# Kernel tuning notes

Hardware: AMD Instinct MI355X
Metric: run time of the kernel (lower is better)

The kernel has to match this reference:

```python
import jax, jax.numpy as jnp
import numpy as np

N, E, F = 20000, 160000, 128
H, C1, C2 = 4, 128, 256
G, NCLS = 64, 10


def setup_inputs() -> dict:
    key = jax.random.key(0)
    ks = jax.random.split(key, 14)
    s = 0.05
    inp = {
        "x": jax.random.normal(ks[0], (N, F), jnp.float32),
        "edge_index": jax.random.randint(ks[1], (2, E), 0, N, dtype=jnp.int32),
        "batch": ((jnp.arange(N, dtype=jnp.int32) * G) // N),  # sorted graph ids, all 64 graphs non-empty
        # GATConv 1: in=128 -> 128 per head, heads=4, concat -> 512
        "W1": jax.random.normal(ks[2], (F, H * C1), jnp.float32) * s,
        "att_src1": jax.random.normal(ks[3], (H, C1), jnp.float32) * s,
        "att_dst1": jax.random.normal(ks[4], (H, C1), jnp.float32) * s,
        "b1": jnp.zeros((H * C1,), jnp.float32),
        # GATConv 2: in=512 -> 256, heads=1, concat=False
        "W2": jax.random.normal(ks[5], (H * C1, C2), jnp.float32) * s,
        "att_src2": jax.random.normal(ks[6], (1, C2), jnp.float32) * s,
        "att_dst2": jax.random.normal(ks[7], (1, C2), jnp.float32) * s,
        "b2": jnp.zeros((C2,), jnp.float32),
        # fc head
        "fc1_w": jax.random.normal(ks[8], (C2, 64), jnp.float32) * s,
        "fc1_b": jnp.zeros((64,), jnp.float32),
        "fc2_w": jax.random.normal(ks[9], (64, NCLS), jnp.float32) * s,
        "fc2_b": jnp.zeros((NCLS,), jnp.float32),
    }
    return inp


def gat_conv(x, src, dst, W, att_src, att_dst, bias, concat):
    """PyG GATConv: per-edge attention + segment softmax over dst + scatter-add."""
    n = x.shape[0]
    h_, c_ = att_src.shape
    h = (x @ W).reshape(n, h_, c_)                    # [N,H,C]
    a_src = jnp.einsum('nhc,hc->nh', h, att_src)       # [N,H]
    a_dst = jnp.einsum('nhc,hc->nh', h, att_dst)       # [N,H]
    e = jax.nn.leaky_relu(a_src[src] + a_dst[dst], negative_slope=0.2)  # [Etot,H]
    e_max = jax.ops.segment_max(e, dst, num_segments=n)
    ee = jnp.exp(e - e_max[dst])
    denom = jax.ops.segment_sum(ee, dst, num_segments=n)
    alpha = ee / denom[dst]                            # [Etot,H]
    out = jax.ops.segment_sum(h[src] * alpha[:, :, None], dst, num_segments=n)  # [N,H,C]
    out = out.reshape(n, h_ * c_) if concat else out.mean(axis=1)
    return out + bias


def reference(x, edge_index, batch, W1, att_src1, att_dst1, b1,
              W2, att_src2, att_dst2, b2, fc1_w, fc1_b, fc2_w, fc2_b):
    n = x.shape[0]
    # to_undirected: both directions; plus self-loops (GATConv add_self_loops=True)
    loops = jnp.arange(n, dtype=edge_index.dtype)
    src = jnp.concatenate([edge_index[0], edge_index[1], loops])
    dst = jnp.concatenate([edge_index[1], edge_index[0], loops])
    h = gat_conv(x, src, dst, W1, att_src1, att_dst1, b1, concat=True)
    h = jax.nn.relu(h)
    h = gat_conv(h, src, dst, W2, att_src2, att_dst2, b2, concat=False)
    g = jax.ops.segment_max(h, batch, num_segments=G)  # global_max_pool
    g = jax.nn.relu(g @ fc1_w + fc1_b) @ fc2_w + fc2_b
    return jax.nn.log_softmax(g, axis=1)
```

## Files before the change

### kernel.cpp

```cpp
#include <hip/hip_runtime.h>
#include <math.h>

#define FDIM 128
#define HEADS 4
#define C1DIM 128
#define C2DIM 256
#define NGRAPH 64
#define NCLS 10

typedef __attribute__((ext_vector_type(8))) short short8;
typedef __attribute__((ext_vector_type(4))) float float4v;
typedef __attribute__((ext_vector_type(2))) float floatx2;

__device__ __forceinline__ unsigned short f2bf(float f) {
    unsigned u = __builtin_bit_cast(unsigned, f);
    unsigned r = (u + 0x7FFFu + ((u >> 16) & 1u)) >> 16;
    return (unsigned short)r;
}
__device__ __forceinline__ float bfu(unsigned short u) { return __builtin_bit_cast(float, (unsigned)u << 16); }
__device__ __forceinline__ float lrelu(float x) { return x > 0.f ? x : 0.2f * x; }
__device__ __forceinline__ float sel4(float a, float b, float c, float d, int hd) {
    return hd == 0 ? a : hd == 1 ? b : hd == 2 ? c : d;
}
__device__ __forceinline__ unsigned char f2fp8(float f) {
    return (unsigned char)(__builtin_amdgcn_cvt_pk_fp8_f32(f, f, 0, false) & 0xff);
}
__device__ __forceinline__ void fp8x8_dec(int2 r, float* f) {
    floatx2 p0 = __builtin_amdgcn_cvt_pk_f32_fp8(r.x, false);
    floatx2 p1 = __builtin_amdgcn_cvt_pk_f32_fp8(r.x, true);
    floatx2 p2 = __builtin_amdgcn_cvt_pk_f32_fp8(r.y, false);
    floatx2 p3 = __builtin_amdgcn_cvt_pk_f32_fp8(r.y, true);
    f[0] = p0.x; f[1] = p0.y; f[2] = p1.x; f[3] = p1.y;
    f[4] = p2.x; f[5] = p2.y; f[6] = p3.x; f[7] = p3.y;
}
__device__ __forceinline__ void fp8x4_dec(int r, float* f) {
    floatx2 p0 = __builtin_amdgcn_cvt_pk_f32_fp8(r, false);
    floatx2 p1 = __builtin_amdgcn_cvt_pk_f32_fp8(r, true);
    f[0] = p0.x; f[1] = p0.y; f[2] = p1.x; f[3] = p1.y;
}
__device__ __forceinline__ unsigned encf(float v) {
    unsigned b = __builtin_bit_cast(unsigned, v);
    return (b & 0x80000000u) ? ~b : (b | 0x80000000u);
}
__device__ __forceinline__ float decf(unsigned u) {
    unsigned b = (u & 0x80000000u) ? (u ^ 0x80000000u) : ~u;
    return __builtin_bit_cast(float, b);
}

__global__ __launch_bounds__(256) void prep_kernel(
        int* __restrict__ zero_base, int nzero_words,
        const float* __restrict__ x, unsigned short* __restrict__ xb, int n4,
        const float* __restrict__ W1, unsigned short* __restrict__ W1t,
        const float* __restrict__ W2, unsigned short* __restrict__ W2t,
        int ZB, int CB) {
    __shared__ float tile[32][33];
    int blk = blockIdx.x;
    if (blk < ZB) {
        int i = blk * 256 + threadIdx.x;
        if (i < nzero_words) zero_base[i] = 0;
        return;
    }
    blk -= ZB;
    if (blk < CB) {
        int i = blk * 256 + threadIdx.x;
        if (i < n4) {
            float4 v = ((const float4*)x)[i];
            ushort4 o;
            o.x = f2bf(v.x); o.y = f2bf(v.y); o.z = f2bf(v.z); o.w = f2bf(v.w);
            ((ushort4*)xb)[i] = o;
        }
        return;
    }
    blk -= CB;
    const float* W; unsigned short* Wt; int K, Nc, bx, by;
    if (blk < 64) {
        W = W1; Wt = W1t; K = 128; Nc = 512;
        bx = (blk & 15) * 32; by = (blk >> 4) * 32;
    } else {
        blk -= 64;
        W = W2; Wt = W2t; K = 512; Nc = 256;
        bx = (blk & 7) * 32; by = (blk >> 3) * 32;
    }
    int tx = threadIdx.x & 31, ty = threadIdx.x >> 5;
    #pragma unroll
    for (int r = 0; r < 32; r += 8)
        tile[ty + r][tx] = W[(size_t)(by + ty + r) * Nc + bx + tx];
    __syncthreads();
    #pragma unroll
    for (int r = 0; r < 32; r += 8)
        Wt[(size_t)(bx + ty + r) * K + by + tx] = f2bf(tile[tx][ty + r]);
}

__global__ void hist_kernel(const int* __restrict__ ei, int E, int* __restrict__ counts) {
    int i = blockIdx.x * blockDim.x + threadIdx.x;
    if (i >= 2 * E) return;
    int dst = (i < E) ? ei[E + i] : ei[i - E];
    atomicAdd(&counts[dst], 1);
}

__global__ __launch_bounds__(1024) void scan_kernel(int* __restrict__ counts_cursor,
                                                    int* __restrict__ ofs, int N) {
    __shared__ int part[1024];
    int t = threadIdx.x;
    int chunk = (N + 1023) / 1024;
    int b = t * chunk;
    int e = b + chunk; if (e > N) e = N;
    int s = 0;
    int i = b;
    if ((chunk & 3) == 0) {
        for (; i + 4 <= e; i += 4) {
            int4 v = *(const int4*)&counts_cursor[i];
            s += v.x + v.y + v.z + v.w;
        }
    }
    for (; i < e; ++i) s += counts_cursor[i];
    part[t] = s;
    __syncthreads();
    for (int o = 1; o < 1024; o <<= 1) {
        int v = (t >= o) ? part[t - o] : 0;
        __syncthreads();
        part[t] += v;
        __syncthreads();
    }
    int run = part[t] - s;
    i = b;
    if ((chunk & 3) == 0) {
        for (; i + 4 <= e; i += 4) {
            int4 c = *(const int4*)&counts_cursor[i];
            int4 o4;
            o4.x = run; run += c.x;
            o4.y = run; run += c.y;
            o4.z = run; run += c.z;
            o4.w = run; run += c.w;
            *(int4*)&ofs[i] = o4;
            counts_cursor[i]     = o4.x;
            counts_cursor[i + 1] = o4.y;
            counts_cursor[i + 2] = o4.z;
            counts_cursor[i + 3] = o4.w;
        }
    }
    for (; i < e; ++i) {
        int c = counts_cursor[i];
        ofs[i] = run;
        counts_cursor[i] = run;
        run += c;
    }
    if (t == 1023) ofs[N] = part[1023];
}

__global__ void scatter_kernel(const int* __restrict__ ei, int E,
                               int* __restrict__ cursor, int* __restrict__ esrc) {
    int i = blockIdx.x * blockDim.x + threadIdx.x;
    if (i >= 2 * E) return;
    int src = ei[i];
    int dst = (i < E) ? ei[E + i] : ei[i - E];
    int pos = atomicAdd(&cursor[dst], 1);
    esrc[pos] = src;
}

template<int MODE>
__global__ __launch_bounds__(256) void bgemm_kernel(
        const unsigned short* __restrict__ A,
        const unsigned short* __restrict__ Bt,
        unsigned char* __restrict__ Cout,
        const float* __restrict__ att_src,
        const float* __restrict__ att_dst,
        float* __restrict__ as_out,
        float* __restrict__ ad_out,
        int M, int N_, int K) {
    constexpr int BN = (MODE == 1) ? 128 : 256;
    constexpr int JW = BN / 32;
    constexpr int CPADB = BN + 16;
    constexpr int SMEMB = 4096 + BN * 64;
    __shared__ __align__(16) unsigned char smem[SMEMB];
    unsigned short* As = (unsigned short*)smem;
    unsigned short* Bs = (unsigned short*)(smem + 4096);
    __shared__ float sd_s[4][32];
    __shared__ float sd_d[4][32];
    const int t = threadIdx.x;
    const int lane = t & 63;
    const int wave = t >> 6;
    const int row0 = blockIdx.y * 64, col0 = blockIdx.x * BN;
    const int wr = (wave >> 1) * 32, wc = (wave & 1) * (BN / 2);
    float4v acc[2][JW] = {};
    for (int k0 = 0; k0 < K; k0 += 32) {
        {
            int i = t;
            int gr = row0 + (i >> 2); if (gr >= M) gr = M - 1;
            const unsigned short* gp = A + (size_t)gr * K + k0 + ((i & 3) << 3);
            __builtin_amdgcn_global_load_lds(
                (const __attribute__((address_space(1))) unsigned int*)gp,
                (__attribute__((address_space(3))) unsigned int*)&As[i * 8], 16, 0, 0);
        }
        #pragma unroll
        for (int c = 0; c < BN / 64; ++c) {
            int i = c * 256 + t;
            int gn = col0 + (i >> 2);
            const unsigned short* gp = Bt + (size_t)gn * K + k0 + ((i & 3) << 3);
            __builtin_amdgcn_global_load_lds(
                (const __attribute__((address_space(1))) unsigned int*)gp,
                (__attribute__((address_space(3))) unsigned int*)&Bs[i * 8], 16, 0, 0);
        }
        __syncthreads();
        short8 af[2], bfr[JW];
        #pragma unroll
        for (int i = 0; i < 2; ++i)
            af[i] = *(const short8*)&As[(wr + i * 16 + (lane & 15)) * 32 + (lane >> 4) * 8];
        #pragma unroll
        for (int j = 0; j < JW; ++j)
            bfr[j] = *(const short8*)&Bs[(wc + j * 16 + (lane & 15)) * 32 + (lane >> 4) * 8];
        #pragma unroll
        for (int i = 0; i < 2; ++i)
            #pragma unroll
            for (int j = 0; j < JW; ++j)
                acc[i][j] = __builtin_amdgcn_mfma_f32_16x16x32_bf16(af[i], bfr[j], acc[i][j], 0, 0, 0);
        __syncthreads();
    }
    float asv[JW], adv[JW];
    #pragma unroll
    for (int j = 0; j < JW; ++j) {
        int cc = col0 + wc + j * 16 + (lane & 15);
        asv[j] = att_src[cc];
        adv[j] = att_dst[cc];
    }
    #pragma unroll
    for (int i = 0; i < 2; ++i) {
        #pragma unroll
        for (int p = 0; p < 4; ++p) {
            int rr = wr + i * 16 + (lane >> 4) * 4 + p;
            float s = 0.f, d = 0.f;
            #pragma unroll
            for (int j = 0; j < JW; ++j) {
                smem[rr * CPADB + wc + j * 16 + (lane & 15)] = f2fp8(acc[i][j][p]);
                s += acc[i][j][p] * asv[j];
                d += acc[i][j][p] * adv[j];
            }
            #pragma unroll
            for (int o = 1; o <= 8; o <<= 1) { s += __shfl_xor(s, o); d += __shfl_xor(d, o); }
            if ((lane & 15) == 0) {
                int ridx = i * 16 + (lane >> 4) * 4 + p;
                sd_s[wave][ridx] = s;
                sd_d[wave][ridx] = d;
            }
        }
    }
    __syncthreads();
    #pragma unroll
    for (int it = 0; it < BN / 64; ++it) {
        int idx = it * 256 + t;
        int row = idx / (BN / 16), c16 = (idx % (BN / 16)) * 16;
        int grw = row0 + row;
        if (grw < M)
            *(int4*)&Cout[(size_t)grw * N_ + col0 + c16] = *(const int4*)&smem[row * CPADB + c16];
    }
    if ((wave & 1) == 0 && lane < 32) {
        float s = sd_s[wave][lane] + sd_s[wave + 1][lane];
        float d = sd_d[wave][lane] + sd_d[wave + 1][lane];
        int r = row0 + wr + lane;
        if (r < M) {
            if (MODE == 1) {
                as_out[r * 4 + blockIdx.x] = s;
                ad_out[r * 4 + blockIdx.x] = d;
            } else {
                as_out[r] = s;
                ad_out[r] = d;
            }
        }
    }
}

__global__ __launch_bounds__(256) void edge_agg1_kernel(
        const unsigned char* __restrict__ h1f8,
        const float4* __restrict__ as14,
        const float4* __restrict__ ad14,
        const int* __restrict__ ofs,
        const int* __restrict__ esrc,
        const float* __restrict__ b1,
        unsigned short* __restrict__ ho1b, int N) {
    __shared__ int sl_s[4][64];
    __shared__ __align__(16) float4 w_s[4][64];
    int wave = threadIdx.x >> 6, lane = threadIdx.x & 63;
    int node = blockIdx.x * 4 + wave;
    if (node >= N) return;
    int beg = ofs[node], end = ofs[node + 1];
    float4 asn = as14[node], adn = ad14[node];
    float w0 = __expf(lrelu(asn.x + adn.x));
    float w1 = __expf(lrelu(asn.y + adn.y));
    float w2 = __expf(lrelu(asn.z + adn.z));
    float w3 = __expf(lrelu(asn.w + adn.w));
    int hd = lane >> 4;
    int c0 = lane * 8;
    float wsh = sel4(w0, w1, w2, w3, hd);
    float acc[8];
    {
        int2 rs = *(const int2*)&h1f8[(size_t)node * 512 + c0];
        float f[8]; fp8x8_dec(rs, f);
        #pragma unroll
        for (int k = 0; k < 8; ++k) acc[k] = wsh * f[k];
    }
    float d0 = 0.f, d1 = 0.f, d2 = 0.f, d3 = 0.f;
    for (int cb = beg; cb < end; cb += 64) {
        int idx = cb + lane;
        int sl = esrc[idx < end ? idx : end - 1];
        float4 wl = make_float4(0.f, 0.f, 0.f, 0.f);
        if (idx < end) {
            float4 a = as14[sl];
            wl.x = __expf(lrelu(a.x + adn.x));
            wl.y = __expf(lrelu(a.y + adn.y));
            wl.z = __expf(lrelu(a.z + adn.z));
            wl.w = __expf(lrelu(a.w + adn.w));
            d0 += wl.x; d1 += wl.y; d2 += wl.z; d3 += wl.w;
        }
        sl_s[wave][lane] = sl;
        w_s[wave][lane] = wl;
        int jmax = end - cb; if (jmax > 64) jmax = 64;
        int j = 0;
        for (; j + 4 <= jmax; j += 4) {
            int s0 = sl_s[wave][j],     s1 = sl_s[wave][j + 1];
            int s2 = sl_s[wave][j + 2], s3 = sl_s[wave][j + 3];
            float u0 = ((const float*)&w_s[wave][j])[hd];
            float u1 = ((const float*)&w_s[wave][j + 1])[hd];
            float u2 = ((const float*)&w_s[wave][j + 2])[hd];
            float u3 = ((const float*)&w_s[wave][j + 3])[hd];
            int2 r0 = *(const int2*)&h1f8[(size_t)s0 * 512 + c0];
            int2 r1 = *(const int2*)&h1f8[(size_t)s1 * 512 + c0];
            int2 r2 = *(const int2*)&h1f8[(size_t)s2 * 512 + c0];
            int2 r3 = *(const int2*)&h1f8[(size_t)s3 * 512 + c0];
            float f0[8], f1[8], f2[8], f3[8];
            fp8x8_dec(r0, f0); fp8x8_dec(r1, f1); fp8x8_dec(r2, f2); fp8x8_dec(r3, f3);
            #pragma unroll
            for (int k = 0; k < 8; ++k)
                acc[k] += u0 * f0[k] + u1 * f1[k] + u2 * f2[k] + u3 * f3[k];
        }
        for (; j < jmax; ++j) {
            int s = sl_s[wave][j];
            float u = ((const float*)&w_s[wave][j])[hd];
            int2 r = *(const int2*)&h1f8[(size_t)s * 512 + c0];
            float f[8]; fp8x8_dec(r, f);
            #pragma unroll
            for (int k = 0; k < 8; ++k) acc[k] += u * f[k];
        }
    }
    #pragma unroll
    for (int o = 32; o > 0; o >>= 1) {
        d0 += __shfl_xor(d0, o); d1 += __shfl_xor(d1, o);
        d2 += __shfl_xor(d2, o); d3 += __shfl_xor(d3, o);
    }
    d0 += w0; d1 += w1; d2 += w2; d3 += w3;
    float dh = sel4(d0, d1, d2, d3, hd);
    float inv = 1.f / dh;
    float4 bA = *(const float4*)&b1[c0], bB = *(const float4*)&b1[c0 + 4];
    float v0 = fmaxf(acc[0] * inv + bA.x, 0.f), v1 = fmaxf(acc[1] * inv + bA.y, 0.f);
    float v2 = fmaxf(acc[2] * inv + bA.z, 0.f), v3 = fmaxf(acc[3] * inv + bA.w, 0.f);
    float v4 = fmaxf(acc[4] * inv + bB.x, 0.f), v5 = fmaxf(acc[5] * inv + bB.y, 0.f);
    float v6 = fmaxf(acc[6] * inv + bB.z, 0.f), v7 = fmaxf(acc[7] * inv + bB.w, 0.f);
    int4 o;
    o.x = (int)((unsigned)f2bf(v0) | ((unsigned)f2bf(v1) << 16));
    o.y = (int)((unsigned)f2bf(v2) | ((unsigned)f2bf(v3) << 16));
    o.z = (int)((unsigned)f2bf(v4) | ((unsigned)f2bf(v5) << 16));
    o.w = (int)((unsigned)f2bf(v6) | ((unsigned)f2bf(v7) << 16));
    *(int4*)&ho1b[(size_t)node * 512 + c0] = o;
}

__global__ __launch_bounds__(256) void edge_agg2_kernel(
        const unsigned char* __restrict__ h2f8,
        const float* __restrict__ as2,
        const float* __restrict__ ad2,
        const int* __restrict__ ofs,
        const int* __restrict__ esrc,
        const float* __restrict__ b2,
        const int* __restrict__ batch,
        unsigned* __restrict__ pool, int N) {
    __shared__ unsigned pms[4][256];
    __shared__ int sl_s[4][64];
    __shared__ float w_s[4][64];
    int wave = threadIdx.x >> 6, lane = threadIdx.x & 63;
    int node = blockIdx.x * 4 + wave;
    bool valid = node < N;
    int c0 = lane * 4;
    unsigned e0 = 0, e1 = 0, e2 = 0, e3 = 0;
    if (valid) {
        int beg = ofs[node], end = ofs[node + 1];
        float adn = ad2[node];
        float wself = __expf(lrelu(as2[node] + adn));
        float a0, a1, a2, a3;
        {
            int r = *(const int*)&h2f8[(size_t)node * 256 + c0];
            float f[4]; fp8x4_dec(r, f);
            a0 = wself * f[0]; a1 = wself * f[1]; a2 = wself * f[2]; a3 = wself * f[3];
        }
        float dsum = 0.f;
        for (int cb = beg; cb < end; cb += 64) {
            int idx = cb + lane;
            int sl = esrc[idx < end ? idx : end - 1];
            float wl = 0.f;
            if (idx < end) {
                wl = __expf(lrelu(as2[sl] + adn));
                dsum += wl;
            }
            sl_s[wave][lane] = sl;
            w_s[wave][lane] = wl;
            int jmax = end - cb; if (jmax > 64) jmax = 64;
            int j = 0;
            for (; j + 8 <= jmax; j += 8) {
                int ss[8]; float u[8]; int r[8];
                #pragma unroll
                for (int q = 0; q < 8; ++q) {
                    ss[q] = sl_s[wave][j + q];
                    u[q] = w_s[wave][j + q];
                }
                #pragma unroll
                for (int q = 0; q < 8; ++q) r[q] = *(const int*)&h2f8[(size_t)ss[q] * 256 + c0];
                #pragma unroll
                for (int q = 0; q < 8; ++q) {
                    float f[4]; fp8x4_dec(r[q], f);
                    a0 += u[q] * f[0]; a1 += u[q] * f[1];
                    a2 += u[q] * f[2]; a3 += u[q] * f[3];
                }
            }
            for (; j < jmax; ++j) {
                int s = sl_s[wave][j];
                float u = w_s[wave][j];
                int r = *(const int*)&h2f8[(size_t)s * 256 + c0];
                float f[4]; fp8x4_dec(r, f);
                a0 += u * f[0]; a1 += u * f[1]; a2 += u * f[2]; a3 += u * f[3];
            }
        }
        #pragma unroll
        for (int o = 32; o > 0; o >>= 1) dsum += __shfl_xor(dsum, o);
        dsum += wself;
        float inv = 1.f / dsum;
        float4 bv = *(const float4*)&b2[c0];
        e0 = encf(a0 * inv + bv.x);
        e1 = encf(a1 * inv + bv.y);
        e2 = encf(a2 * inv + bv.z);
        e3 = encf(a3 * inv + bv.w);
    }
    pms[wave][c0]     = e0;
    pms[wave][c0 + 1] = e1;
    pms[wave][c0 + 2] = e2;
    pms[wave][c0 + 3] = e3;
    __syncthreads();
    int n0 = blockIdx.x * 4;
    int n3 = n0 + 3; if (n3 >= N) n3 = N - 1;
    int g0 = batch[n0], g3 = batch[n3];
    if (g0 == g3) {
        int tt = threadIdx.x;
        unsigned m0 = pms[0][tt] > pms[1][tt] ? pms[0][tt] : pms[1][tt];
        unsigned m1 = pms[2][tt] > pms[3][tt] ? pms[2][tt] : pms[3][tt];
        unsigned m = m0 > m1 ? m0 : m1;
        atomicMax(&pool[(size_t)g0 * 256 + tt], m);
    } else if (valid) {
        int g = batch[node];
        atomicMax(&pool[(size_t)g * 256 + c0], e0);
        atomicMax(&pool[(size_t)g * 256 + c0 + 1], e1);
        atomicMax(&pool[(size_t)g * 256 + c0 + 2], e2);
        atomicMax(&pool[(size_t)g * 256 + c0 + 3], e3);
    }
}

__global__ __launch_bounds__(64) void head_kernel(const unsigned* __restrict__ pool,
                                                  const float* __restrict__ fc1w,
                                                  const float* __restrict__ fc1b,
                                                  const float* __restrict__ fc2w,
                                                  const float* __restrict__ fc2b,
                                                  float* __restrict__ out) {
    __shared__ float gr[256];
    __shared__ float hid[64];
    __shared__ float o10[NCLS];
    int g = blockIdx.x, t = threadIdx.x;
    for (int i = t; i < 256; i += 64)
        gr[i] = decf(pool[(size_t)g * 256 + i]);
    __syncthreads();
    float s = fc1b[t];
    for (int k = 0; k < 256; ++k) s += gr[k] * fc1w[k * 64 + t];
    hid[t] = s > 0.f ? s : 0.f;
    __syncthreads();
    if (t < NCLS) {
        float s2 = fc2b[t];
        for (int k = 0; k < 64; ++k) s2 += hid[k] * fc2w[k * NCLS + t];
        o10[t] = s2;
    }
    __syncthreads();
    if (t == 0) {
        float mx = -INFINITY;
        for (int c = 0; c < NCLS; ++c) mx = fmaxf(mx, o10[c]);
        float se = 0.f;
        for (int c = 0; c < NCLS; ++c) se += __expf(o10[c] - mx);
        float lse = mx + logf(se);
        for (int c = 0; c < NCLS; ++c) out[g * NCLS + c] = o10[c] - lse;
    }
}

extern "C" void kernel_launch(void* const* d_in, const int* in_sizes, int n_in,
                              void* d_out, int out_size, void* d_ws, size_t ws_size,
                              hipStream_t stream) {
    (void)n_in; (void)out_size; (void)ws_size;
    const float* x        = (const float*)d_in[0];
    const int*   ei       = (const int*)d_in[1];
    const int*   batch    = (const int*)d_in[2];
    const float* W1       = (const float*)d_in[3];
    const float* att_src1 = (const float*)d_in[4];
    const float* att_dst1 = (const float*)d_in[5];
    const float* b1       = (const float*)d_in[6];
    const float* W2       = (const float*)d_in[7];
    const float* att_src2 = (const float*)d_in[8];
    const float* att_dst2 = (const float*)d_in[9];
    const float* b2       = (const float*)d_in[10];
    const float* fc1w     = (const float*)d_in[11];
    const float* fc1b     = (const float*)d_in[12];
    const float* fc2w     = (const float*)d_in[13];
    const float* fc2b     = (const float*)d_in[14];

    const int N = in_sizes[2];
    const int E = in_sizes[1] / 2;
    const int tot = 2 * E;

    char* base = (char*)d_ws;
    size_t off = 0;
    auto alloc = [&](size_t bytes) -> void* {
        void* p = base + off;
        off = (off + bytes + 255) & ~(size_t)255;
        return p;
    };
    int*      ofs    = (int*)alloc((size_t)(N + 1) * 4);
    int*      cursor = (int*)alloc((size_t)N * 4);
    unsigned* pool   = (unsigned*)alloc((size_t)NGRAPH * 256 * 4);
    size_t zend = off;
    int*   esrc   = (int*)alloc((size_t)tot * 4);
    float* as1    = (float*)alloc((size_t)N * HEADS * 4);
    float* ad1    = (float*)alloc((size_t)N * HEADS * 4);
    float* as2    = (float*)alloc((size_t)N * 4);
    float* ad2    = (float*)alloc((size_t)N * 4);
    unsigned short* xb   = (unsigned short*)alloc((size_t)N * FDIM * 2);
    unsigned short* W1t  = (unsigned short*)alloc((size_t)512 * 128 * 2);
    unsigned short* W2t  = (unsigned short*)alloc((size_t)256 * 512 * 2);
    unsigned char*  h1f8 = (unsigned char*)alloc((size_t)N * 512);
    unsigned short* ho1b = (unsigned short*)alloc((size_t)N * 512 * 2);
    unsigned char*  h2f8 = (unsigned char*)alloc((size_t)N * 256);

    int nzero = (int)((zend - (size_t)((char*)cursor - base)) / 4);
    int ZB = (nzero + 255) / 256;
    int n4 = N * FDIM / 4;
    int CB = (n4 + 255) / 256;
    prep_kernel<<<ZB + CB + 64 + 128, 256, 0, stream>>>(
        cursor, nzero, x, xb, n4, W1, W1t, W2, W2t, ZB, CB);

    hist_kernel<<<(tot + 255) / 256, 256, 0, stream>>>(ei, E, cursor);
    scan_kernel<<<1, 1024, 0, stream>>>(cursor, ofs, N);
    scatter_kernel<<<(tot + 255) / 256, 256, 0, stream>>>(ei, E, cursor, esrc);

    bgemm_kernel<1><<<dim3(4, (N + 63) / 64), 256, 0, stream>>>(
        xb, W1t, h1f8, att_src1, att_dst1, as1, ad1, N, 512, 128);
    edge_agg1_kernel<<<(N + 3) / 4, 256, 0, stream>>>(h1f8, (const float4*)as1, (const float4*)ad1,
                                                      ofs, esrc, b1, ho1b, N);

    bgemm_kernel<2><<<dim3(1, (N + 63) / 64), 256, 0, stream>>>(
        ho1b, W2t, h2f8, att_src2, att_dst2, as2, ad2, N, 256, 512);
    edge_agg2_kernel<<<(N + 3) / 4, 256, 0, stream>>>(h2f8, as2, ad2, ofs, esrc, b2,
                                                      batch, pool, N);

    head_kernel<<<NGRAPH, 64, 0, stream>>>(pool, fc1w, fc1b, fc2w, fc2b, (float*)d_out);
}
```

Baseline: 228.0 us.

## Merge prep, histogram and scan into fewer launches, overlapping scan with GEMM1

```diff
diff --git a/kernel.cpp b/kernel.cpp
--- a/kernel.cpp
+++ b/kernel.cpp
@@ -47,12 +47,11 @@
     return __builtin_bit_cast(float, b);
 }
 
-__global__ __launch_bounds__(256) void prep_kernel(
+__global__ __launch_bounds__(256) void zerotc_kernel(
         int* __restrict__ zero_base, int nzero_words,
-        const float* __restrict__ x, unsigned short* __restrict__ xb, int n4,
         const float* __restrict__ W1, unsigned short* __restrict__ W1t,
         const float* __restrict__ W2, unsigned short* __restrict__ W2t,
-        int ZB, int CB) {
+        int ZB) {
     __shared__ float tile[32][33];
     int blk = blockIdx.x;
     if (blk < ZB) {
@@ -61,17 +60,6 @@
         return;
     }
     blk -= ZB;
-    if (blk < CB) {
-        int i = blk * 256 + threadIdx.x;
-        if (i < n4) {
-            float4 v = ((const float4*)x)[i];
-            ushort4 o;
-            o.x = f2bf(v.x); o.y = f2bf(v.y); o.z = f2bf(v.z); o.w = f2bf(v.w);
-            ((ushort4*)xb)[i] = o;
-        }
-        return;
-    }
-    blk -= CB;
     const float* W; unsigned short* Wt; int K, Nc, bx, by;
     if (blk < 64) {
         W = W1; Wt = W1t; K = 128; Nc = 512;
@@ -91,61 +79,67 @@
         Wt[(size_t)(bx + ty + r) * K + by + tx] = f2bf(tile[tx][ty + r]);
 }
 
-__global__ void hist_kernel(const int* __restrict__ ei, int E, int* __restrict__ counts) {
-    int i = blockIdx.x * blockDim.x + threadIdx.x;
-    if (i >= 2 * E) return;
-    int dst = (i < E) ? ei[E + i] : ei[i - E];
-    atomicAdd(&counts[dst], 1);
-}
-
-__global__ __launch_bounds__(1024) void scan_kernel(int* __restrict__ counts_cursor,
-                                                    int* __restrict__ ofs, int N) {
-    __shared__ int part[1024];
+__global__ __launch_bounds__(256) void prep2_kernel(
+        const float* __restrict__ x, unsigned short* __restrict__ xb, int n4,
+        const int* __restrict__ ei, int E, int* __restrict__ cursor, int CB) {
+    int blk = blockIdx.x;
+    if (blk < CB) {
+        int i = blk * 256 + threadIdx.x;
+        if (i < n4) {
+            float4 v = ((const float4*)x)[i];
+            ushort4 o;
+            o.x = f2bf(v.x); o.y = f2bf(v.y); o.z = f2bf(v.z); o.w = f2bf(v.w);
+            ((ushort4*)xb)[i] = o;
+        }
+        return;
+    }
+    int i = (blk - CB) * 256 + threadIdx.x;
+    if (i < 2 * E) {
+        int dst = (i < E) ? ei[E + i] : ei[i - E];
+        atomicAdd(&cursor[dst], 1);
+    }
+}
+
+__device__ __forceinline__ void scan_block256(int* __restrict__ cnt, int* __restrict__ ofs, int N) {
+    __shared__ int spart[256];
     int t = threadIdx.x;
-    int chunk = (N + 1023) / 1024;
+    int chunk = (((N + 255) / 256) + 3) & ~3;
     int b = t * chunk;
     int e = b + chunk; if (e > N) e = N;
     int s = 0;
     int i = b;
-    if ((chunk & 3) == 0) {
-        for (; i + 4 <= e; i += 4) {
-            int4 v = *(const int4*)&counts_cursor[i];
-            s += v.x + v.y + v.z + v.w;
-        }
-    }
-    for (; i < e; ++i) s += counts_cursor[i];
-    part[t] = s;
-    __syncthreads();
-    for (int o = 1; o < 1024; o <<= 1) {
-        int v = (t >= o) ? part[t - o] : 0;
+    for (; i + 4 <= e; i += 4) {
+        int4 v = *(const int4*)&cnt[i];
+        s += v.x + v.y + v.z + v.w;
+    }
+    for (; i < e; ++i) s += cnt[i];
+    spart[t] = s;
+    __syncthreads();
+    for (int o = 1; o < 256; o <<= 1) {
+        int v = (t >= o) ? spart[t - o] : 0;
         __syncthreads();
-        part[t] += v;
+        spart[t] += v;
         __syncthreads();
     }
-    int run = part[t] - s;
+    int run = spart[t] - s;
     i = b;
-    if ((chunk & 3) == 0) {
-        for (; i + 4 <= e; i += 4) {
-            int4 c = *(const int4*)&counts_cursor[i];
-            int4 o4;
-            o4.x = run; run += c.x;
-            o4.y = run; run += c.y;
-            o4.z = run; run += c.z;
-            o4.w = run; run += c.w;
-            *(int4*)&ofs[i] = o4;
-            counts_cursor[i]     = o4.x;
-            counts_cursor[i + 1] = o4.y;
-            counts_cursor[i + 2] = o4.z;
-            counts_cursor[i + 3] = o4.w;
-        }
+    for (; i + 4 <= e; i += 4) {
+        int4 c = *(const int4*)&cnt[i];
+        int4 o4;
+        o4.x = run; run += c.x;
+        o4.y = run; run += c.y;
+        o4.z = run; run += c.z;
+        o4.w = run; run += c.w;
+        *(int4*)&ofs[i] = o4;
+        *(int4*)&cnt[i] = o4;
     }
     for (; i < e; ++i) {
-        int c = counts_cursor[i];
+        int c = cnt[i];
         ofs[i] = run;
-        counts_cursor[i] = run;
+        cnt[i] = run;
         run += c;
     }
-    if (t == 1023) ofs[N] = part[1023];
+    if (t == 255) ofs[N] = spart[255];
 }
 
 __global__ void scatter_kernel(const int* __restrict__ ei, int E,
@@ -167,7 +161,12 @@
         const float* __restrict__ att_dst,
         float* __restrict__ as_out,
         float* __restrict__ ad_out,
-        int M, int N_, int K) {
+        int M, int N_, int K,
+        int* __restrict__ scan_cnt, int* __restrict__ scan_ofs, int Nnodes) {
+    if (MODE == 1 && blockIdx.x == 0) {
+        scan_block256(scan_cnt, scan_ofs, Nnodes);
+        return;
+    }
     constexpr int BN = (MODE == 1) ? 128 : 256;
     constexpr int JW = BN / 32;
     constexpr int CPADB = BN + 16;
@@ -180,7 +179,17 @@
     const int t = threadIdx.x;
     const int lane = t & 63;
     const int wave = t >> 6;
-    const int row0 = blockIdx.y * 64, col0 = blockIdx.x * BN;
+    int row0, col0, headi;
+    if (MODE == 1) {
+        int bb = blockIdx.x - 1;
+        headi = bb & 3;
+        col0 = headi * BN;
+        row0 = (bb >> 2) * 64;
+    } else {
+        headi = 0;
+        col0 = 0;
+        row0 = blockIdx.x * 64;
+    }
     const int wr = (wave >> 1) * 32, wc = (wave & 1) * (BN / 2);
     float4v acc[2][JW] = {};
     for (int k0 = 0; k0 < K; k0 += 32) {
@@ -259,8 +268,8 @@
         int r = row0 + wr + lane;
         if (r < M) {
             if (MODE == 1) {
-                as_out[r * 4 + blockIdx.x] = s;
-                ad_out[r * 4 + blockIdx.x] = d;
+                as_out[r * 4 + headi] = s;
+                ad_out[r * 4 + headi] = d;
             } else {
                 as_out[r] = s;
                 ad_out[r] = d;
@@ -541,22 +550,25 @@
 
     int nzero = (int)((zend - (size_t)((char*)cursor - base)) / 4);
     int ZB = (nzero + 255) / 256;
+    zerotc_kernel<<<ZB + 64 + 128, 256, 0, stream>>>(cursor, nzero, W1, W1t, W2, W2t, ZB);
+
     int n4 = N * FDIM / 4;
     int CB = (n4 + 255) / 256;
-    prep_kernel<<<ZB + CB + 64 + 128, 256, 0, stream>>>(
-        cursor, nzero, x, xb, n4, W1, W1t, W2, W2t, ZB, CB);
-
-    hist_kernel<<<(tot + 255) / 256, 256, 0, stream>>>(ei, E, cursor);
-    scan_kernel<<<1, 1024, 0, stream>>>(cursor, ofs, N);
-    scatter_kernel<<<(tot + 255) / 256, 256, 0, stream>>>(ei, E, cursor, esrc);
-
-    bgemm_kernel<1><<<dim3(4, (N + 63) / 64), 256, 0, stream>>>(
-        xb, W1t, h1f8, att_src1, att_dst1, as1, ad1, N, 512, 128);
+    int HB = (tot + 255) / 256;
+    prep2_kernel<<<CB + HB, 256, 0, stream>>>(x, xb, n4, ei, E, cursor, CB);
+
+    int rowb = (N + 63) / 64;
+    bgemm_kernel<1><<<1 + 4 * rowb, 256, 0, stream>>>(
+        xb, W1t, h1f8, att_src1, att_dst1, as1, ad1, N, 512, 128, cursor, ofs, N);
+
+    scatter_kernel<<<HB, 256, 0, stream>>>(ei, E, cursor, esrc);
+
     edge_agg1_kernel<<<(N + 3) / 4, 256, 0, stream>>>(h1f8, (const float4*)as1, (const float4*)ad1,
                                                       ofs, esrc, b1, ho1b, N);
 
-    bgemm_kernel<2><<<dim3(1, (N + 63) / 64), 256, 0, stream>>>(
-        ho1b, W2t, h2f8, att_src2, att_dst2, as2, ad2, N, 256, 512);
+    bgemm_kernel<2><<<rowb, 256, 0, stream>>>(
+        ho1b, W2t, h2f8, att_src2, att_dst2, as2, ad2, N, 256, 512, nullptr, nullptr, 0);
+
     edge_agg2_kernel<<<(N + 3) / 4, 256, 0, stream>>>(h2f8, as2, ad2, ofs, esrc, b2,
                                                       batch, pool, N);
 
```

After: 224.9 us. No clear change (-1.4%).
